# Kernel optimization log

Measured on AMD Instinct MI355X. Metric: run time of the kernel, lower is better.

The kernel has to match this reference:

```python
import jax, jax.numpy as jnp
import numpy as np

BS, D, D_WM, W, H = 1024, 1024, 256, 512, 8
HD = D_WM // H
SCALE = 1.0 / np.sqrt(HD)


def setup_inputs() -> dict:
    key = jax.random.key(0)
    ks = jax.random.split(key, 12)
    inp = {
        'x': jax.random.normal(ks[0], (BS, D), jnp.float32),
        'wm_K': jax.random.normal(ks[1], (BS, W, D_WM), jnp.float32),
        'wm_V': jax.random.normal(ks[2], (BS, W, D_WM), jnp.float32),
        'Wq_w': jax.random.normal(ks[3], (D_WM, D), jnp.float32) * 0.02,
        'Wq_b': jnp.zeros((D_WM,), jnp.float32),
        'Wk_w': jax.random.normal(ks[4], (D_WM, D), jnp.float32) * 0.02,
        'Wk_b': jnp.zeros((D_WM,), jnp.float32),
        'Wv_w': jax.random.normal(ks[5], (D_WM, D), jnp.float32) * 0.02,
        'Wv_b': jnp.zeros((D_WM,), jnp.float32),
        'Wo_w': jax.random.normal(ks[6], (D, D_WM), jnp.float32) * 0.02,
        'Wo_b': jnp.zeros((D,), jnp.float32),
        'reset_mask': jnp.zeros((BS,), bool),
        'wm_valid': jnp.ones((BS, W), bool),
        'wm_ptr': jax.random.randint(ks[7], (BS,), 0, W, jnp.int32).astype(jnp.int64),
    }
    return inp


def reference(x, wm_K, wm_V, Wq_w, Wq_b, Wk_w, Wk_b, Wv_w, Wv_b, Wo_w, Wo_b,
              reset_mask, wm_valid, wm_ptr):
    # --- doc-boundary reset ---
    keep = ~reset_mask                              # [BS]
    valid = wm_valid & keep[:, None]                # [BS, W]
    ptr = jnp.where(keep, wm_ptr, 0).astype(jnp.int32)  # [BS]

    # --- projections ---
    q = x @ Wq_w.T + Wq_b                           # [BS, D_wm]
    k = x @ Wk_w.T + Wk_b
    v = x @ Wv_w.T + Wv_b

    # --- ring-buffer scatter write at ptr (one-hot blend, grad path) ---
    m = jax.nn.one_hot(ptr, W, dtype=wm_K.dtype)[:, :, None]  # [BS, W, 1]
    K = wm_K * (1.0 - m) + k[:, None, :] * m        # [BS, W, D_wm]
    V = wm_V * (1.0 - m) + v[:, None, :] * m
    slot = jnp.arange(W)
    valid = valid | (slot[None, :] == ptr[:, None])  # written slot now valid

    # --- single-query attention over W slots ---
    q_h = q.reshape(BS, H, HD)
    K_h = K.reshape(BS, W, H, HD)
    V_h = V.reshape(BS, W, H, HD)
    attn = jnp.einsum('bhd,bwhd->bhw', q_h, K_h) * SCALE  # [BS, H, W]

    # ALiBi recency bias: age of slot j = (ptr - j) % W
    slopes = 2.0 ** (-8.0 * jnp.arange(1, H + 1, dtype=jnp.float32) / H)
    dist = jnp.mod(ptr[:, None] - slot[None, :], W).astype(jnp.float32)  # [BS, W]
    attn = attn + (-slopes[None, :, None]) * dist[:, None, :]

    attn = jnp.where(valid[:, None, :], attn, -jnp.inf)
    all_invalid = ~jnp.any(valid, axis=-1)          # [BS]
    p = jax.nn.softmax(attn, axis=-1)
    p = jnp.where(all_invalid[:, None, None], 0.0, p)

    out = jnp.einsum('bhw,bwhd->bhd', p, V_h).reshape(BS, D_WM)
    y_wm = out @ Wo_w.T + Wo_b                      # [BS, D]
    return y_wm
```

## Files before the change

### kernel.cpp

```cpp
#include <hip/hip_runtime.h>


#define BSZ   1024
#define DIM   1024
#define DWM   256
#define WSL   512
#define NH    8

typedef _Float16 half8 __attribute__((ext_vector_type(8)));
typedef float    floatx4 __attribute__((ext_vector_type(4)));

constexpr float SCALE_ = 0.17677669529663687f;
constexpr float LOG2E_ = 1.4426950408889634f;

__global__ __launch_bounds__(256) void k_convert(
    const float* __restrict__ x,
    const float* __restrict__ wq, const float* __restrict__ wk,
    const float* __restrict__ wv, const float* __restrict__ wo,
    const float* __restrict__ bq, const float* __restrict__ bk,
    const float* __restrict__ bv,
    const void* __restrict__ validraw, const void* __restrict__ ptrraw,
    _Float16* __restrict__ xh, _Float16* __restrict__ wh,
    _Float16* __restrict__ woh, float* __restrict__ biasc,
    int* __restrict__ flags)
{
    const int i = blockIdx.x * 256 + threadIdx.x;
    const int e = i * 4;

    const float* src;
    _Float16* dst;
    if (e < 1048576) {
        src = x + e;       dst = xh + e;
    } else if (e < 1835008) {
        const int e2 = e - 1048576;
        src = (e2 < 262144) ? (wq + e2)
            : (e2 < 524288) ? (wk + (e2 - 262144))
                            : (wv + (e2 - 524288));
        dst = wh + e2;
    } else {
        const int e3 = e - 1835008;
        src = wo + e3;     dst = woh + e3;
    }
    const float4 f = *(const float4*)src;
    dst[0] = (_Float16)f.x; dst[1] = (_Float16)f.y;
    dst[2] = (_Float16)f.z; dst[3] = (_Float16)f.w;

    if (i < 192) {
        const int j = i * 4;
        #pragma unroll
        for (int u = 0; u < 4; ++u) {
            const int jj = j + u;
            biasc[jj] = (jj < 256) ? bq[jj] : (jj < 512) ? bk[jj - 256] : bv[jj - 512];
        }
    }

    if (i == 0) {
        const unsigned int w0 = *(const unsigned int*)validraw;
        flags[0] = (w0 == 0x01010101u) ? 1 : 0;
        const int* p32 = (const int*)ptrraw;
        int is64 = 1, nz = 0;
        #pragma unroll
        for (int t = 0; t < 32; t += 2) {
            if (p32[t + 1] != 0) is64 = 0;
            if (p32[t] != 0) nz = 1;
        }
        flags[1] = (is64 && nz) ? 1 : 0;
    }
}

template<int KK, int LDC>
__global__ __launch_bounds__(256) void k_gemm_nt(
    const _Float16* __restrict__ A, const _Float16* __restrict__ B,
    const float* __restrict__ bias, float* __restrict__ C)
{
    const int lane = threadIdx.x & 63;
    const int wave = threadIdx.x >> 6;
    const int m0 = blockIdx.x * 64 + wave * 16;
    const int n0 = blockIdx.y * 32;
    const int r  = lane & 15;
    const int kg = lane >> 4;

    const _Float16* ap  = A + (size_t)(m0 + r) * KK + kg * 8;
    const _Float16* bp0 = B + (size_t)(n0 + r) * KK + kg * 8;
    const _Float16* bp1 = bp0 + (size_t)16 * KK;

    floatx4 acc0 = {0.f, 0.f, 0.f, 0.f};
    floatx4 acc1 = {0.f, 0.f, 0.f, 0.f};
    #pragma unroll 4
    for (int kt = 0; kt < KK / 32; ++kt) {
        half8 a  = *(const half8*)(ap  + kt * 32);
        half8 b0 = *(const half8*)(bp0 + kt * 32);
        half8 b1 = *(const half8*)(bp1 + kt * 32);
        acc0 = __builtin_amdgcn_mfma_f32_16x16x32_f16(a, b0, acc0, 0, 0, 0);
        acc1 = __builtin_amdgcn_mfma_f32_16x16x32_f16(a, b1, acc1, 0, 0, 0);
    }

    const int col0 = n0 + r;
    const int col1 = n0 + 16 + r;
    const float bn0 = bias[col0];
    const float bn1 = bias[col1];
    #pragma unroll
    for (int i = 0; i < 4; ++i) {
        const int row = m0 + kg * 4 + i;
        C[(size_t)row * LDC + col0] = acc0[i] + bn0;
        C[(size_t)row * LDC + col1] = acc1[i] + bn1;
    }
}

__global__ __launch_bounds__(256) void k_attn(
    const float* __restrict__ qkv,
    const float* __restrict__ wmK,
    const float* __restrict__ wmV,
    const void* __restrict__ resetraw,
    const void* __restrict__ validraw,
    const void* __restrict__ ptrraw,
    const int* __restrict__ flags,
    _Float16* __restrict__ outh)
{
    const int b    = blockIdx.x;
    const int tid  = threadIdx.x;
    const int lane = tid & 63;
    const int wave = tid >> 6;
    const int h    = lane >> 3;

    const int bytelay = flags[0];
    const int ptr64   = flags[1];

    bool keep;
    if (bytelay) keep = (((const unsigned char*)resetraw)[b] == 0);
    else         keep = (((const int*)resetraw)[b] == 0);
    int ptr = ptr64 ? ((const int*)ptrraw)[2 * b] : ((const int*)ptrraw)[b];
    if (!keep) ptr = 0;

    __shared__ float bias_s[WSL * NH];
    __shared__ float accS[4 * 64 * 4];
    __shared__ float lS[4 * 64];

    const unsigned char* vb = (const unsigned char*)validraw;
    const int* vi = (const int*)validraw;
    for (int idx = tid; idx < WSL * NH; idx += 256) {
        const int s  = idx >> 3;
        const int hh = idx & 7;
        const float slope2 = exp2f(-(float)(hh + 1)) * LOG2E_;
        const int dist = (ptr - s) & (WSL - 1);
        float bb = -slope2 * (float)dist;
        const bool vok = bytelay ? (vb[b * WSL + s] != 0) : (vi[b * WSL + s] != 0);
        if (!(vok && keep) || s == ptr) bb = -1e30f;
        bias_s[idx] = bb;
    }

    const float4 q4 = *(const float4*)(qkv + b * 768 + lane * 4);
    const float4 k4 = *(const float4*)(qkv + b * 768 + 256 + lane * 4);
    const float4 v4 = *(const float4*)(qkv + b * 768 + 512 + lane * 4);

    __syncthreads();

    const float C1 = SCALE_ * LOG2E_;
    float lsum = 0.f;
    float4 acc = {0.f, 0.f, 0.f, 0.f};

    const floatx4* Kp = (const floatx4*)wmK + (size_t)b * WSL * 64 + lane;
    const floatx4* Vp = (const floatx4*)wmV + (size_t)b * WSL * 64 + lane;
    const int s0 = wave * 128;

    #pragma unroll 8
    for (int s = s0; s < s0 + 128; ++s) {
        const floatx4 kk = __builtin_nontemporal_load(Kp + s * 64);
        float t = q4.x * kk[0] + q4.y * kk[1] + q4.z * kk[2] + q4.w * kk[3];
        t += __shfl_xor(t, 1);
        t += __shfl_xor(t, 2);
        t += __shfl_xor(t, 4);
        const float p = exp2f(fmaf(t, C1, bias_s[s * 8 + h]));
        lsum += p;
        const floatx4 vv = __builtin_nontemporal_load(Vp + s * 64);
        acc.x = fmaf(p, vv[0], acc.x);
        acc.y = fmaf(p, vv[1], acc.y);
        acc.z = fmaf(p, vv[2], acc.z);
        acc.w = fmaf(p, vv[3], acc.w);
    }

    *(float4*)(accS + (wave * 64 + lane) * 4) = acc;
    lS[wave * 64 + lane] = lsum;
    __syncthreads();

    if (tid < 64) {
        float4 A = {0.f, 0.f, 0.f, 0.f};
        float L = 0.f;
        #pragma unroll
        for (int w2 = 0; w2 < 4; ++w2) {
            const float4 aw = *(const float4*)(accS + (w2 * 64 + lane) * 4);
            A.x += aw.x; A.y += aw.y; A.z += aw.z; A.w += aw.w;
            L += lS[w2 * 64 + lane];
        }
        float t = q4.x * k4.x + q4.y * k4.y + q4.z * k4.z + q4.w * k4.w;
        t += __shfl_xor(t, 1);
        t += __shfl_xor(t, 2);
        t += __shfl_xor(t, 4);
        const float p = exp2f(t * C1);
        L += p;
        A.x = fmaf(p, v4.x, A.x);
        A.y = fmaf(p, v4.y, A.y);
        A.z = fmaf(p, v4.z, A.z);
        A.w = fmaf(p, v4.w, A.w);

        const float inv = 1.0f / L;
        _Float16* op = outh + b * 256 + lane * 4;
        op[0] = (_Float16)(A.x * inv);
        op[1] = (_Float16)(A.y * inv);
        op[2] = (_Float16)(A.z * inv);
        op[3] = (_Float16)(A.w * inv);
    }
}

extern "C" void kernel_launch(void* const* d_in, const int* in_sizes, int n_in,
                              void* d_out, int out_size, void* d_ws, size_t ws_size,
                              hipStream_t stream)
{
    const float* x   = (const float*)d_in[0];
    const float* wmK = (const float*)d_in[1];
    const float* wmV = (const float*)d_in[2];
    const float* Wq  = (const float*)d_in[3];
    const float* bq  = (const float*)d_in[4];
    const float* Wk  = (const float*)d_in[5];
    const float* bk  = (const float*)d_in[6];
    const float* Wv  = (const float*)d_in[7];
    const float* bv  = (const float*)d_in[8];
    const float* Wo  = (const float*)d_in[9];
    const float* bo  = (const float*)d_in[10];
    const void* reset = d_in[11];
    const void* valid = d_in[12];
    const void* ptr   = d_in[13];
    float* y = (float*)d_out;

    char* ws = (char*)d_ws;
    _Float16* xh   = (_Float16*)(ws);
    _Float16* wh   = (_Float16*)(ws + 2097152);
    _Float16* woh  = (_Float16*)(ws + 3670016);
    float*    qkv  = (float*)   (ws + 4194304);
    _Float16* outh = (_Float16*)(ws + 7340032);
    float*    biasc= (float*)   (ws + 7864320);
    int*      flags= (int*)     (ws + 7867392);

    k_convert<<<2048, 256, 0, stream>>>(x, Wq, Wk, Wv, Wo, bq, bk, bv,
                                        valid, ptr, xh, wh, woh, biasc, flags);
    k_gemm_nt<1024, 768><<<dim3(16, 24), 256, 0, stream>>>(xh, wh, biasc, qkv);
    k_attn<<<1024, 256, 0, stream>>>(qkv, wmK, wmV, reset, valid, ptr, flags, outh);
    k_gemm_nt<256, 1024><<<dim3(16, 32), 256, 0, stream>>>(outh, woh, bo, y);
}
```

Baseline: 204.2 us.

## Fuse fp16 conversion into GEMMs and split attention across two blocks per row

Drops the separate fp32-to-fp16 conversion kernel: both GEMMs now load fp32 inputs and weights and convert in registers before the MFMA, and the layout-detection flags are recomputed inside the attention kernel. Attention is split into two blocks per batch row, each covering half the slots, with a small combine kernel that merges the partial sums and adds the new-slot term. This removes one kernel pass and its fp16 staging traffic, and doubles the block count for the bandwidth-bound attention. In exchange the GEMMs read twice as many bytes per operand and convert repeatedly, and an extra launch plus partial-result traffic is added.

```diff
diff --git a/kernel.cpp b/kernel.cpp
--- a/kernel.cpp
+++ b/kernel.cpp
@@ -2,76 +2,33 @@
 
 
 #define BSZ   1024
-#define DIM   1024
-#define DWM   256
 #define WSL   512
 #define NH    8
 
-typedef _Float16 half8 __attribute__((ext_vector_type(8)));
-typedef float    floatx4 __attribute__((ext_vector_type(4)));
+typedef _Float16 half8  __attribute__((ext_vector_type(8)));
+typedef float   floatx4 __attribute__((ext_vector_type(4)));
 
 constexpr float SCALE_ = 0.17677669529663687f;
 constexpr float LOG2E_ = 1.4426950408889634f;
 
-__global__ __launch_bounds__(256) void k_convert(
+__device__ inline half8 ldcvt8(const float* __restrict__ p) {
+    const floatx4 a = *(const floatx4*)p;
+    const floatx4 b = *(const floatx4*)(p + 4);
+    half8 h;
+    h[0] = (_Float16)a[0]; h[1] = (_Float16)a[1];
+    h[2] = (_Float16)a[2]; h[3] = (_Float16)a[3];
+    h[4] = (_Float16)b[0]; h[5] = (_Float16)b[1];
+    h[6] = (_Float16)b[2]; h[7] = (_Float16)b[3];
+    return h;
+}
+
+__global__ __launch_bounds__(256) void k_qkv(
     const float* __restrict__ x,
     const float* __restrict__ wq, const float* __restrict__ wk,
-    const float* __restrict__ wv, const float* __restrict__ wo,
+    const float* __restrict__ wv,
     const float* __restrict__ bq, const float* __restrict__ bk,
     const float* __restrict__ bv,
-    const void* __restrict__ validraw, const void* __restrict__ ptrraw,
-    _Float16* __restrict__ xh, _Float16* __restrict__ wh,
-    _Float16* __restrict__ woh, float* __restrict__ biasc,
-    int* __restrict__ flags)
-{
-    const int i = blockIdx.x * 256 + threadIdx.x;
-    const int e = i * 4;
-
-    const float* src;
-    _Float16* dst;
-    if (e < 1048576) {
-        src = x + e;       dst = xh + e;
-    } else if (e < 1835008) {
-        const int e2 = e - 1048576;
-        src = (e2 < 262144) ? (wq + e2)
-            : (e2 < 524288) ? (wk + (e2 - 262144))
-                            : (wv + (e2 - 524288));
-        dst = wh + e2;
-    } else {
-        const int e3 = e - 1835008;
-        src = wo + e3;     dst = woh + e3;
-    }
-    const float4 f = *(const float4*)src;
-    dst[0] = (_Float16)f.x; dst[1] = (_Float16)f.y;
-    dst[2] = (_Float16)f.z; dst[3] = (_Float16)f.w;
-
-    if (i < 192) {
-        const int j = i * 4;
-        #pragma unroll
-        for (int u = 0; u < 4; ++u) {
-            const int jj = j + u;
-            biasc[jj] = (jj < 256) ? bq[jj] : (jj < 512) ? bk[jj - 256] : bv[jj - 512];
-        }
-    }
-
-    if (i == 0) {
-        const unsigned int w0 = *(const unsigned int*)validraw;
-        flags[0] = (w0 == 0x01010101u) ? 1 : 0;
-        const int* p32 = (const int*)ptrraw;
-        int is64 = 1, nz = 0;
-        #pragma unroll
-        for (int t = 0; t < 32; t += 2) {
-            if (p32[t + 1] != 0) is64 = 0;
-            if (p32[t] != 0) nz = 1;
-        }
-        flags[1] = (is64 && nz) ? 1 : 0;
-    }
-}
-
-template<int KK, int LDC>
-__global__ __launch_bounds__(256) void k_gemm_nt(
-    const _Float16* __restrict__ A, const _Float16* __restrict__ B,
-    const float* __restrict__ bias, float* __restrict__ C)
+    float* __restrict__ qkv)
 {
     const int lane = threadIdx.x & 63;
     const int wave = threadIdx.x >> 6;
@@ -80,51 +37,65 @@
     const int r  = lane & 15;
     const int kg = lane >> 4;
 
-    const _Float16* ap  = A + (size_t)(m0 + r) * KK + kg * 8;
-    const _Float16* bp0 = B + (size_t)(n0 + r) * KK + kg * 8;
-    const _Float16* bp1 = bp0 + (size_t)16 * KK;
+    const int seg = n0 >> 8;
+    const float* W  = (seg == 0) ? wq : (seg == 1) ? wk : wv;
+    const float* bb = (seg == 0) ? bq : (seg == 1) ? bk : bv;
+    const int nr = (n0 & 255) + r;
+
+    const float* ap  = x + (size_t)(m0 + r) * 1024 + kg * 8;
+    const float* bp0 = W + (size_t)nr * 1024 + kg * 8;
+    const float* bp1 = bp0 + (size_t)16 * 1024;
 
     floatx4 acc0 = {0.f, 0.f, 0.f, 0.f};
     floatx4 acc1 = {0.f, 0.f, 0.f, 0.f};
     #pragma unroll 4
-    for (int kt = 0; kt < KK / 32; ++kt) {
-        half8 a  = *(const half8*)(ap  + kt * 32);
-        half8 b0 = *(const half8*)(bp0 + kt * 32);
-        half8 b1 = *(const half8*)(bp1 + kt * 32);
+    for (int kt = 0; kt < 32; ++kt) {
+        const half8 a  = ldcvt8(ap  + kt * 32);
+        const half8 b0 = ldcvt8(bp0 + kt * 32);
+        const half8 b1 = ldcvt8(bp1 + kt * 32);
         acc0 = __builtin_amdgcn_mfma_f32_16x16x32_f16(a, b0, acc0, 0, 0, 0);
         acc1 = __builtin_amdgcn_mfma_f32_16x16x32_f16(a, b1, acc1, 0, 0, 0);
     }
 
     const int col0 = n0 + r;
-    const int col1 = n0 + 16 + r;
-    const float bn0 = bias[col0];
-    const float bn1 = bias[col1];
+    const float bn0 = bb[(n0 & 255) + r];
+    const float bn1 = bb[(n0 & 255) + 16 + r];
     #pragma unroll
     for (int i = 0; i < 4; ++i) {
         const int row = m0 + kg * 4 + i;
-        C[(size_t)row * LDC + col0] = acc0[i] + bn0;
-        C[(size_t)row * LDC + col1] = acc1[i] + bn1;
-    }
-}
-
-__global__ __launch_bounds__(256) void k_attn(
+        qkv[(size_t)row * 768 + col0]      = acc0[i] + bn0;
+        qkv[(size_t)row * 768 + col0 + 16] = acc1[i] + bn1;
+    }
+}
+
+__global__ __launch_bounds__(256) void k_attn_part(
     const float* __restrict__ qkv,
     const float* __restrict__ wmK,
     const float* __restrict__ wmV,
     const void* __restrict__ resetraw,
     const void* __restrict__ validraw,
     const void* __restrict__ ptrraw,
-    const int* __restrict__ flags,
-    _Float16* __restrict__ outh)
-{
-    const int b    = blockIdx.x;
+    float* __restrict__ pacc,
+    float* __restrict__ pl)
+{
+    const int blk  = blockIdx.x;
+    const int b    = blk >> 1;
+    const int sbase = (blk & 1) * 256;
     const int tid  = threadIdx.x;
     const int lane = tid & 63;
     const int wave = tid >> 6;
     const int h    = lane >> 3;
 
-    const int bytelay = flags[0];
-    const int ptr64   = flags[1];
+    const unsigned int w0 = *(const unsigned int*)validraw;
+    const int bytelay = (w0 == 0x01010101u) ? 1 : 0;
+    const int* p32 = (const int*)ptrraw;
+    int is64 = 1, nz = 0;
+    #pragma unroll
+    for (int t = 0; t < 32; t += 2) {
+        if (p32[t + 1] != 0) is64 = 0;
+        if (p32[t] != 0) nz = 1;
+    }
+    const int ptr64 = (is64 && nz) ? 1 : 0;
 
     bool keep;
     if (bytelay) keep = (((const unsigned char*)resetraw)[b] == 0);
@@ -132,14 +103,15 @@
     int ptr = ptr64 ? ((const int*)ptrraw)[2 * b] : ((const int*)ptrraw)[b];
     if (!keep) ptr = 0;
 
-    __shared__ float bias_s[WSL * NH];
+    __shared__ float bias_s[256 * NH];
     __shared__ float accS[4 * 64 * 4];
     __shared__ float lS[4 * 64];
 
     const unsigned char* vb = (const unsigned char*)validraw;
     const int* vi = (const int*)validraw;
-    for (int idx = tid; idx < WSL * NH; idx += 256) {
-        const int s  = idx >> 3;
+    for (int idx = tid; idx < 256 * NH; idx += 256) {
+        const int sl = idx >> 3;
+        const int s  = sbase + sl;
         const int hh = idx & 7;
         const float slope2 = exp2f(-(float)(hh + 1)) * LOG2E_;
         const int dist = (ptr - s) & (WSL - 1);
@@ -150,9 +122,6 @@
     }
 
     const float4 q4 = *(const float4*)(qkv + b * 768 + lane * 4);
-    const float4 k4 = *(const float4*)(qkv + b * 768 + 256 + lane * 4);
-    const float4 v4 = *(const float4*)(qkv + b * 768 + 512 + lane * 4);
-
     __syncthreads();
 
     const float C1 = SCALE_ * LOG2E_;
@@ -161,16 +130,16 @@
 
     const floatx4* Kp = (const floatx4*)wmK + (size_t)b * WSL * 64 + lane;
     const floatx4* Vp = (const floatx4*)wmV + (size_t)b * WSL * 64 + lane;
-    const int s0 = wave * 128;
+    const int s0 = sbase + wave * 64;
 
     #pragma unroll 8
-    for (int s = s0; s < s0 + 128; ++s) {
+    for (int s = s0; s < s0 + 64; ++s) {
         const floatx4 kk = __builtin_nontemporal_load(Kp + s * 64);
         float t = q4.x * kk[0] + q4.y * kk[1] + q4.z * kk[2] + q4.w * kk[3];
         t += __shfl_xor(t, 1);
         t += __shfl_xor(t, 2);
         t += __shfl_xor(t, 4);
-        const float p = exp2f(fmaf(t, C1, bias_s[s * 8 + h]));
+        const float p = exp2f(fmaf(t, C1, bias_s[(s - sbase) * 8 + h]));
         lsum += p;
         const floatx4 vv = __builtin_nontemporal_load(Vp + s * 64);
         acc.x = fmaf(p, vv[0], acc.x);
@@ -192,23 +161,82 @@
             A.x += aw.x; A.y += aw.y; A.z += aw.z; A.w += aw.w;
             L += lS[w2 * 64 + lane];
         }
-        float t = q4.x * k4.x + q4.y * k4.y + q4.z * k4.z + q4.w * k4.w;
-        t += __shfl_xor(t, 1);
-        t += __shfl_xor(t, 2);
-        t += __shfl_xor(t, 4);
-        const float p = exp2f(t * C1);
-        L += p;
-        A.x = fmaf(p, v4.x, A.x);
-        A.y = fmaf(p, v4.y, A.y);
-        A.z = fmaf(p, v4.z, A.z);
-        A.w = fmaf(p, v4.w, A.w);
-
-        const float inv = 1.0f / L;
-        _Float16* op = outh + b * 256 + lane * 4;
-        op[0] = (_Float16)(A.x * inv);
-        op[1] = (_Float16)(A.y * inv);
-        op[2] = (_Float16)(A.z * inv);
-        op[3] = (_Float16)(A.w * inv);
+        *(float4*)(pacc + (size_t)blk * 256 + lane * 4) = A;
+        pl[blk * 64 + lane] = L;
+    }
+}
+
+__global__ __launch_bounds__(256) void k_attn_comb(
+    const float* __restrict__ qkv,
+    const float* __restrict__ pacc, const float* __restrict__ pl,
+    _Float16* __restrict__ outh)
+{
+    const int tid  = threadIdx.x;
+    const int lane = tid & 63;
+    const int b    = blockIdx.x * 4 + (tid >> 6);
+
+    const float4 a0 = *(const float4*)(pacc + (size_t)(2 * b)     * 256 + lane * 4);
+    const float4 a1 = *(const float4*)(pacc + (size_t)(2 * b + 1) * 256 + lane * 4);
+    float4 A = {a0.x + a1.x, a0.y + a1.y, a0.z + a1.z, a0.w + a1.w};
+    float L = pl[(2 * b) * 64 + lane] + pl[(2 * b + 1) * 64 + lane];
+
+    const float4 q4 = *(const float4*)(qkv + b * 768 + lane * 4);
+    const float4 k4 = *(const float4*)(qkv + b * 768 + 256 + lane * 4);
+    const float4 v4 = *(const float4*)(qkv + b * 768 + 512 + lane * 4);
+
+    float t = q4.x * k4.x + q4.y * k4.y + q4.z * k4.z + q4.w * k4.w;
+    t += __shfl_xor(t, 1);
+    t += __shfl_xor(t, 2);
+    t += __shfl_xor(t, 4);
+    const float p = exp2f(t * SCALE_ * LOG2E_);
+    L += p;
+    A.x = fmaf(p, v4.x, A.x);
+    A.y = fmaf(p, v4.y, A.y);
+    A.z = fmaf(p, v4.z, A.z);
+    A.w = fmaf(p, v4.w, A.w);
+
+    const float inv = 1.0f / L;
+    _Float16* op = outh + b * 256 + lane * 4;
+    op[0] = (_Float16)(A.x * inv);
+    op[1] = (_Float16)(A.y * inv);
+    op[2] = (_Float16)(A.z * inv);
+    op[3] = (_Float16)(A.w * inv);
+}
+
+__global__ __launch_bounds__(256) void k_out(
+    const _Float16* __restrict__ A, const float* __restrict__ Wo,
+    const float* __restrict__ bo, float* __restrict__ C)
+{
+    const int lane = threadIdx.x & 63;
+    const int wave = threadIdx.x >> 6;
+    const int m0 = blockIdx.x * 64 + wave * 16;
+    const int n0 = blockIdx.y * 32;
+    const int r  = lane & 15;
+    const int kg = lane >> 4;
+
+    const _Float16* ap = A + (size_t)(m0 + r) * 256 + kg * 8;
+    const float* bp0 = Wo + (size_t)(n0 + r) * 256 + kg * 8;
+    const float* bp1 = bp0 + (size_t)16 * 256;
+
+    floatx4 acc0 = {0.f, 0.f, 0.f, 0.f};
+    floatx4 acc1 = {0.f, 0.f, 0.f, 0.f};
+    #pragma unroll
+    for (int kt = 0; kt < 8; ++kt) {
+        const half8 a  = *(const half8*)(ap + kt * 32);
+        const half8 b0 = ldcvt8(bp0 + kt * 32);
+        const half8 b1 = ldcvt8(bp1 + kt * 32);
+        acc0 = __builtin_amdgcn_mfma_f32_16x16x32_f16(a, b0, acc0, 0, 0, 0);
+        acc1 = __builtin_amdgcn_mfma_f32_16x16x32_f16(a, b1, acc1, 0, 0, 0);
+    }
+
+    const int col0 = n0 + r;
+    const float bn0 = bo[col0];
+    const float bn1 = bo[col0 + 16];
+    #pragma unroll
+    for (int i = 0; i < 4; ++i) {
+        const int row = m0 + kg * 4 + i;
+        C[(size_t)row * 1024 + col0]      = acc0[i] + bn0;
+        C[(size_t)row * 1024 + col0 + 16] = acc1[i] + bn1;
     }
 }
 
@@ -233,17 +261,13 @@
     float* y = (float*)d_out;
 
     char* ws = (char*)d_ws;
-    _Float16* xh   = (_Float16*)(ws);
-    _Float16* wh   = (_Float16*)(ws + 2097152);
-    _Float16* woh  = (_Float16*)(ws + 3670016);
-    float*    qkv  = (float*)   (ws + 4194304);
-    _Float16* outh = (_Float16*)(ws + 7340032);
-    float*    biasc= (float*)   (ws + 7864320);
-    int*      flags= (int*)     (ws + 7867392);
-
-    k_convert<<<2048, 256, 0, stream>>>(x, Wq, Wk, Wv, Wo, bq, bk, bv,
-                                        valid, ptr, xh, wh, woh, biasc, flags);
-    k_gemm_nt<1024, 768><<<dim3(16, 24), 256, 0, stream>>>(xh, wh, biasc, qkv);
-    k_attn<<<1024, 256, 0, stream>>>(qkv, wmK, wmV, reset, valid, ptr, flags, outh);
-    k_gemm_nt<256, 1024><<<dim3(16, 32), 256, 0, stream>>>(outh, woh, bo, y);
-}
+    float*    qkv  = (float*)   (ws);
+    _Float16* outh = (_Float16*)(ws + 3145728);
+    float*    pacc = (float*)   (ws + 3670016);
+    float*    pl   = (float*)   (ws + 5767168);
+
+    k_qkv<<<dim3(16, 24), 256, 0, stream>>>(x, Wq, Wk, Wv, bq, bk, bv, qkv);
+    k_attn_part<<<2048, 256, 0, stream>>>(qkv, wmK, wmV, reset, valid, ptr, pacc, pl);
+    k_attn_comb<<<256, 256, 0, stream>>>(qkv, pacc, pl, outh);
+    k_out<<<dim3(16, 32), 256, 0, stream>>>(outh, Wo, bo, y);
+}
```

Result: slower. 247.6 us (+21.2%).

## Split attention over slot halves into partial blocks plus a combine kernel

Applied to the files above, without the earlier changes.

The attention kernel is split so each batch row is handled by two blocks, each covering half of the ring-buffer slots. Each block writes partial accumulators and softmax denominators to workspace. A new combine kernel adds the two halves, includes the freshly written slot and normalizes. The aim is more blocks and memory-level parallelism for the bandwidth-bound K/V streaming, at the cost of an extra launch and a round trip of the partial results through workspace.

```diff
diff --git a/kernel.cpp b/kernel.cpp
--- a/kernel.cpp
+++ b/kernel.cpp
@@ -2,13 +2,11 @@
 
 
 #define BSZ   1024
-#define DIM   1024
-#define DWM   256
 #define WSL   512
 #define NH    8
 
-typedef _Float16 half8 __attribute__((ext_vector_type(8)));
-typedef float    floatx4 __attribute__((ext_vector_type(4)));
+typedef _Float16 half8  __attribute__((ext_vector_type(8)));
+typedef float   floatx4 __attribute__((ext_vector_type(4)));
 
 constexpr float SCALE_ = 0.17677669529663687f;
 constexpr float LOG2E_ = 1.4426950408889634f;
@@ -107,7 +105,7 @@
     }
 }
 
-__global__ __launch_bounds__(256) void k_attn(
+__global__ __launch_bounds__(256) void k_attn_part(
     const float* __restrict__ qkv,
     const float* __restrict__ wmK,
     const float* __restrict__ wmV,
@@ -115,13 +113,16 @@
     const void* __restrict__ validraw,
     const void* __restrict__ ptrraw,
     const int* __restrict__ flags,
-    _Float16* __restrict__ outh)
-{
-    const int b    = blockIdx.x;
-    const int tid  = threadIdx.x;
-    const int lane = tid & 63;
-    const int wave = tid >> 6;
-    const int h    = lane >> 3;
+    float* __restrict__ pacc,
+    float* __restrict__ pl)
+{
+    const int blk   = blockIdx.x;
+    const int b     = blk >> 1;
+    const int sbase = (blk & 1) * 256;
+    const int tid   = threadIdx.x;
+    const int lane  = tid & 63;
+    const int wave  = tid >> 6;
+    const int h     = lane >> 3;
 
     const int bytelay = flags[0];
     const int ptr64   = flags[1];
@@ -132,14 +133,14 @@
     int ptr = ptr64 ? ((const int*)ptrraw)[2 * b] : ((const int*)ptrraw)[b];
     if (!keep) ptr = 0;
 
-    __shared__ float bias_s[WSL * NH];
+    __shared__ float bias_s[256 * NH];
     __shared__ float accS[4 * 64 * 4];
     __shared__ float lS[4 * 64];
 
     const unsigned char* vb = (const unsigned char*)validraw;
     const int* vi = (const int*)validraw;
-    for (int idx = tid; idx < WSL * NH; idx += 256) {
-        const int s  = idx >> 3;
+    for (int idx = tid; idx < 256 * NH; idx += 256) {
+        const int s  = sbase + (idx >> 3);
         const int hh = idx & 7;
         const float slope2 = exp2f(-(float)(hh + 1)) * LOG2E_;
         const int dist = (ptr - s) & (WSL - 1);
@@ -150,8 +151,6 @@
     }
 
     const float4 q4 = *(const float4*)(qkv + b * 768 + lane * 4);
-    const float4 k4 = *(const float4*)(qkv + b * 768 + 256 + lane * 4);
-    const float4 v4 = *(const float4*)(qkv + b * 768 + 512 + lane * 4);
 
     __syncthreads();
 
@@ -161,16 +160,16 @@
 
     const floatx4* Kp = (const floatx4*)wmK + (size_t)b * WSL * 64 + lane;
     const floatx4* Vp = (const floatx4*)wmV + (size_t)b * WSL * 64 + lane;
-    const int s0 = wave * 128;
+    const int s0 = sbase + wave * 64;
 
     #pragma unroll 8
-    for (int s = s0; s < s0 + 128; ++s) {
+    for (int s = s0; s < s0 + 64; ++s) {
         const floatx4 kk = __builtin_nontemporal_load(Kp + s * 64);
         float t = q4.x * kk[0] + q4.y * kk[1] + q4.z * kk[2] + q4.w * kk[3];
         t += __shfl_xor(t, 1);
         t += __shfl_xor(t, 2);
         t += __shfl_xor(t, 4);
-        const float p = exp2f(fmaf(t, C1, bias_s[s * 8 + h]));
+        const float p = exp2f(fmaf(t, C1, bias_s[(s - sbase) * 8 + h]));
         lsum += p;
         const floatx4 vv = __builtin_nontemporal_load(Vp + s * 64);
         acc.x = fmaf(p, vv[0], acc.x);
@@ -192,24 +191,46 @@
             A.x += aw.x; A.y += aw.y; A.z += aw.z; A.w += aw.w;
             L += lS[w2 * 64 + lane];
         }
-        float t = q4.x * k4.x + q4.y * k4.y + q4.z * k4.z + q4.w * k4.w;
-        t += __shfl_xor(t, 1);
-        t += __shfl_xor(t, 2);
-        t += __shfl_xor(t, 4);
-        const float p = exp2f(t * C1);
-        L += p;
-        A.x = fmaf(p, v4.x, A.x);
-        A.y = fmaf(p, v4.y, A.y);
-        A.z = fmaf(p, v4.z, A.z);
-        A.w = fmaf(p, v4.w, A.w);
-
-        const float inv = 1.0f / L;
-        _Float16* op = outh + b * 256 + lane * 4;
-        op[0] = (_Float16)(A.x * inv);
-        op[1] = (_Float16)(A.y * inv);
-        op[2] = (_Float16)(A.z * inv);
-        op[3] = (_Float16)(A.w * inv);
-    }
+        *(float4*)(pacc + (size_t)blk * 256 + lane * 4) = A;
+        pl[blk * 64 + lane] = L;
+    }
+}
+
+__global__ __launch_bounds__(256) void k_attn_comb(
+    const float* __restrict__ qkv,
+    const float* __restrict__ pacc, const float* __restrict__ pl,
+    _Float16* __restrict__ outh)
+{
+    const int tid  = threadIdx.x;
+    const int lane = tid & 63;
+    const int b    = blockIdx.x * 4 + (tid >> 6);
+
+    const float4 a0 = *(const float4*)(pacc + (size_t)(2 * b)     * 256 + lane * 4);
+    const float4 a1 = *(const float4*)(pacc + (size_t)(2 * b + 1) * 256 + lane * 4);
+    float4 A = {a0.x + a1.x, a0.y + a1.y, a0.z + a1.z, a0.w + a1.w};
+    float L = pl[(2 * b) * 64 + lane] + pl[(2 * b + 1) * 64 + lane];
+
+    const float4 q4 = *(const float4*)(qkv + b * 768 + lane * 4);
+    const float4 k4 = *(const float4*)(qkv + b * 768 + 256 + lane * 4);
+    const float4 v4 = *(const float4*)(qkv + b * 768 + 512 + lane * 4);
+
+    float t = q4.x * k4.x + q4.y * k4.y + q4.z * k4.z + q4.w * k4.w;
+    t += __shfl_xor(t, 1);
+    t += __shfl_xor(t, 2);
+    t += __shfl_xor(t, 4);
+    const float p = exp2f(t * SCALE_ * LOG2E_);
+    L += p;
+    A.x = fmaf(p, v4.x, A.x);
+    A.y = fmaf(p, v4.y, A.y);
+    A.z = fmaf(p, v4.z, A.z);
+    A.w = fmaf(p, v4.w, A.w);
+
+    const float inv = 1.0f / L;
+    _Float16* op = outh + b * 256 + lane * 4;
+    op[0] = (_Float16)(A.x * inv);
+    op[1] = (_Float16)(A.y * inv);
+    op[2] = (_Float16)(A.z * inv);
+    op[3] = (_Float16)(A.w * inv);
 }
 
 extern "C" void kernel_launch(void* const* d_in, const int* in_sizes, int n_in,
@@ -240,10 +261,13 @@
     _Float16* outh = (_Float16*)(ws + 7340032);
     float*    biasc= (float*)   (ws + 7864320);
     int*      flags= (int*)     (ws + 7867392);
+    float*    pacc = (float*)   (ws + 7868416);
+    float*    pl   = (float*)   (ws + 9965568);
 
     k_convert<<<2048, 256, 0, stream>>>(x, Wq, Wk, Wv, Wo, bq, bk, bv,
                                         valid, ptr, xh, wh, woh, biasc, flags);
     k_gemm_nt<1024, 768><<<dim3(16, 24), 256, 0, stream>>>(xh, wh, biasc, qkv);
-    k_attn<<<1024, 256, 0, stream>>>(qkv, wmK, wmV, reset, valid, ptr, flags, outh);
+    k_attn_part<<<2048, 256, 0, stream>>>(qkv, wmK, wmV, reset, valid, ptr, flags, pacc, pl);
+    k_attn_comb<<<256, 256, 0, stream>>>(qkv, pacc, pl, outh);
     k_gemm_nt<256, 1024><<<dim3(16, 32), 256, 0, stream>>>(outh, woh, bo, y);
 }
```

Result: slower. 218.7 us (+7.1%).
